# Kernel optimization log

Hardware: AMD Instinct MI355X
Metric: run time of the kernel (lower is better)

Reference implementation:

```python
import jax, jax.numpy as jnp
import numpy as np

SELF_OBS_DIM = 18
NBR_OBS_DIM = 6
NUM_NBR = 8
HID = 128

def _mlp2(x, W1, b1, W2, b2):
    return jnp.tanh(jnp.tanh(x @ W1 + b1) @ W2 + b2)

def setup_inputs() -> dict:
    key = jax.random.key(0)
    ks = jax.random.split(key, 20)
    B = 65536
    def w(k, i, o):
        return (jax.random.normal(k, (i, o), jnp.float32) / np.sqrt(i)).astype(jnp.float32)
    inp = {
        "self_obs": jax.random.normal(ks[0], (B, SELF_OBS_DIM), jnp.float32),
        "obs": jax.random.normal(ks[1], (B, SELF_OBS_DIM + NUM_NBR * NBR_OBS_DIM), jnp.float32),
        # embedding_mlp
        "e_W1": w(ks[2], SELF_OBS_DIM + NBR_OBS_DIM, HID), "e_b1": jnp.zeros((HID,), jnp.float32),
        "e_W2": w(ks[3], HID, HID), "e_b2": jnp.zeros((HID,), jnp.float32),
        # neighbor_value_mlp
        "v_W1": w(ks[4], HID, HID), "v_b1": jnp.zeros((HID,), jnp.float32),
        "v_W2": w(ks[5], HID, HID), "v_b2": jnp.zeros((HID,), jnp.float32),
        # attention_mlp
        "a_W1": w(ks[6], 2 * HID, HID), "a_b1": jnp.zeros((HID,), jnp.float32),
        "a_W2": w(ks[7], HID, HID), "a_b2": jnp.zeros((HID,), jnp.float32),
        "a_W3": w(ks[8], HID, 1), "a_b3": jnp.zeros((1,), jnp.float32),
        "all_neighbor_obs_size": NUM_NBR * NBR_OBS_DIM,
        "batch_size": B,
    }
    return inp

def reference(self_obs, obs, e_W1, e_b1, e_W2, e_b2, v_W1, v_b1, v_W2, v_b2,
              a_W1, a_b1, a_W2, a_b2, a_W3, a_b3, all_neighbor_obs_size, batch_size):
    B = batch_size
    n = NUM_NBR
    # slice out neighbor obs; reshape is batch-major: row index = b*n + k
    obs_nb = obs[:, SELF_OBS_DIM:SELF_OBS_DIM + all_neighbor_obs_size].reshape(-1, NBR_OBS_DIM)
    # torch .repeat(n, 1) tiles whole batch -> neighbor-major: row index = k*B + b (kept faithful)
    self_rep = jnp.tile(self_obs, (n, 1))
    emb = _mlp2(jnp.concatenate([self_rep, obs_nb], axis=1), e_W1, e_b1, e_W2, e_b2)  # [B*n, H]
    vals = _mlp2(emb, v_W1, v_b1, v_W2, v_b2)                                          # [B*n, H]
    emb_mean = emb.reshape(B, n, HID).mean(axis=1)                                     # [B, H]
    mean_rep = jnp.tile(emb_mean, (n, 1))                                              # [B*n, H]
    h = jnp.tanh(jnp.concatenate([emb, mean_rep], axis=1) @ a_W1 + a_b1)
    h = jnp.tanh(h @ a_W2 + a_b2)
    scores = (h @ a_W3 + a_b3).reshape(B, n)
    attn = jax.nn.softmax(scores, axis=1).reshape(-1, 1)
    out = (attn * vals).reshape(B, n, HID).sum(axis=1)                                 # [B, H]
    return out
```

## Files before the change

### kernel.cpp

```cpp
#include <hip/hip_runtime.h>
#include <math.h>

#define BATCH 65536
#define HID   128
#define NTHREADS 256

using bf16x8 = __attribute__((ext_vector_type(8))) short;
using f32x4  = __attribute__((ext_vector_type(4))) float;

#define E1H 0
#define E1L 4096
#define SWB 8192
#define BIASF 204800
#define MEANH 206592
#define WS_ELEMS_FULL (MEANH + BATCH*HID)

__device__ __forceinline__ float4 ld4(const float* p) { return *reinterpret_cast<const float4*>(p); }

__device__ __forceinline__ unsigned cvtpk(float a, float b) {
    unsigned r;
    asm("v_cvt_pk_bf16_f32 %0, %1, %2" : "=v"(r) : "v"(a), "v"(b));
    return r;
}

__device__ __forceinline__ float tanh_f(float x) {
    float t = __builtin_amdgcn_exp2f(x * 2.8853900817779268f);
    float r = __builtin_amdgcn_rcpf(t + 1.f);
    return 1.f - 2.f * r;
}

__device__ __forceinline__ f32x4 mfma16(bf16x8 a, bf16x8 b, f32x4 c) {
    return __builtin_amdgcn_mfma_f32_16x16x32_bf16(a, b, c, 0, 0, 0);
}

__device__ __forceinline__ bf16x8 pk8(unsigned u0, unsigned u1, unsigned u2, unsigned u3) {
    union { unsigned u[4]; bf16x8 v; } x;
    x.u[0] = u0; x.u[1] = u1; x.u[2] = u2; x.u[3] = u3;
    return x.v;
}

__device__ __forceinline__ void split_pack(float v0, float v1, float v2, float v3,
        unsigned& uh0, unsigned& uh1, unsigned& ul0, unsigned& ul1) {
    uh0 = cvtpk(v0, v1); uh1 = cvtpk(v2, v3);
    float f0 = __uint_as_float(uh0 << 16), f1 = __uint_as_float(uh0 & 0xffff0000u);
    float f2 = __uint_as_float(uh1 << 16), f3 = __uint_as_float(uh1 & 0xffff0000u);
    ul0 = cvtpk(v0 - f0, v1 - f1); ul1 = cvtpk(v2 - f2, v3 - f3);
}

__device__ __forceinline__ void zacc(f32x4 acc[2][8]) {
    #pragma unroll
    for (int rt = 0; rt < 2; ++rt)
        #pragma unroll
        for (int t = 0; t < 8; ++t) acc[rt][t] = f32x4{0.f, 0.f, 0.f, 0.f};
}

__device__ __forceinline__ int permc(int p) {
    return 32 * ((p >> 4) & 3) + 8 * ((p >> 2) & 3) + 4 * (p >> 6) + (p & 3);
}

__device__ __forceinline__ void gload16(const void* g, void* l) {
    __builtin_amdgcn_global_load_lds(
        (const __attribute__((address_space(1))) void*)g,
        (__attribute__((address_space(3))) void*)l, 16, 0, 0);
}
__device__ __forceinline__ void stage16k(short* dst, const short* __restrict__ src, int tid) {
    const char* g = (const char*)src + tid * 16;
    char* l = (char*)dst + tid * 16;
    #pragma unroll
    for (int s = 0; s < 4; ++s) gload16(g + s * 4096, l + s * 4096);
}
__device__ __forceinline__ void stage32k(short* dst, const short* __restrict__ src, int tid) {
    const char* g = (const char*)src + tid * 16;
    char* l = (char*)dst + tid * 16;
    #pragma unroll
    for (int s = 0; s < 8; ++s) gload16(g + s * 4096, l + s * 4096);
}

template<int NMUL, int TPH>
__device__ __forceinline__ void mm_q(f32x4 acc[2][8],
        const bf16x8 Bh[2][4], const bf16x8 Bl[2][4],
        const short* Wq, int sE, int sO)
{
    #pragma unroll
    for (int tp = 0; tp < 2; ++tp) {
        const int t0 = 4 * TPH + 2 * tp, t1 = t0 + 1;
        #pragma unroll
        for (int ks = 0; ks < 4; ++ks) {
            const int base = ((ks & 1) ? sO : sE) + (ks >> 1) * 64 + tp * 4096;
            bf16x8 w0 = *(const bf16x8*)(Wq + base);
            bf16x8 w1 = *(const bf16x8*)(Wq + base + 2048);
            __builtin_amdgcn_s_setprio(1);
            acc[0][t0] = mfma16(w0, Bh[0][ks], acc[0][t0]);
            acc[0][t1] = mfma16(w1, Bh[0][ks], acc[0][t1]);
            acc[1][t0] = mfma16(w0, Bh[1][ks], acc[1][t0]);
            acc[1][t1] = mfma16(w1, Bh[1][ks], acc[1][t1]);
            if (NMUL == 2) {
                acc[0][t0] = mfma16(w0, Bl[0][ks], acc[0][t0]);
                acc[0][t1] = mfma16(w1, Bl[0][ks], acc[0][t1]);
                acc[1][t0] = mfma16(w0, Bl[1][ks], acc[1][t0]);
                acc[1][t1] = mfma16(w1, Bl[1][ks], acc[1][t1]);
            }
            __builtin_amdgcn_s_setprio(0);
        }
    }
}

template<int NH>
__device__ __forceinline__ void layer4(f32x4 acc[2][8],
        const bf16x8 Bh[2][4], const bf16x8 Bl[2][4],
        short* B0, short* B1, const short* __restrict__ src,
        const short* __restrict__ next, int sE, int sO, int tid)
{
    stage16k(B1, src + 8192, tid);
    mm_q<NH, 0>(acc, Bh, Bl, B0, sE, sO);
    __syncthreads();
    stage16k(B0, src + 16384, tid);
    mm_q<NH, 1>(acc, Bh, Bl, B1, sE, sO);
    __syncthreads();
    stage16k(B1, src + 24576, tid);
    mm_q<1, 0>(acc, Bh, Bh, B0, sE, sO);
    __syncthreads();
    if (next) stage16k(B0, next, tid);
    mm_q<1, 1>(acc, Bh, Bh, B1, sE, sO);
}

template<int NMUL>
__device__ __forceinline__ void mm_half(f32x4 acc[2][8],
        const bf16x8 Bh[2][4], const bf16x8 Bl[2][4],
        const short* W, int sE, int sO)
{
    #pragma unroll
    for (int tp = 0; tp < 4; ++tp) {
        const int t0 = 2 * tp, t1 = t0 + 1;
        __builtin_amdgcn_s_setprio(1);
        #pragma unroll
        for (int ks = 0; ks < 4; ++ks) {
            const int base = ((ks & 1) ? sO : sE) + (ks >> 1) * 64 + tp * 4096;
            bf16x8 w0 = *(const bf16x8*)(W + base);
            bf16x8 w1 = *(const bf16x8*)(W + base + 2048);
            acc[0][t0] = mfma16(w0, Bh[0][ks], acc[0][t0]);
            acc[0][t1] = mfma16(w1, Bh[0][ks], acc[0][t1]);
            acc[1][t0] = mfma16(w0, Bh[1][ks], acc[1][t0]);
            acc[1][t1] = mfma16(w1, Bh[1][ks], acc[1][t1]);
            if (NMUL == 2) {
                acc[0][t0] = mfma16(w0, Bl[0][ks], acc[0][t0]);
                acc[0][t1] = mfma16(w1, Bl[0][ks], acc[0][t1]);
                acc[1][t0] = mfma16(w0, Bl[1][ks], acc[1][t0]);
                acc[1][t1] = mfma16(w1, Bl[1][ks], acc[1][t1]);
            }
        }
        __builtin_amdgcn_s_setprio(0);
    }
}

__device__ __forceinline__ void mm_l1(f32x4 acc[2][8],
        const bf16x8 X0h[2], const bf16x8 X0l[2],
        const short* __restrict__ Wh, const short* __restrict__ Wl, int wb)
{
    #pragma unroll
    for (int tp = 0; tp < 4; ++tp) {
        const short* whp = Wh + wb + tp * 1024;
        const short* wlp = Wl + wb + tp * 1024;
        bf16x8 wh0 = *(const bf16x8*)(whp);
        bf16x8 wh1 = *(const bf16x8*)(whp + 512);
        bf16x8 wl0 = *(const bf16x8*)(wlp);
        bf16x8 wl1 = *(const bf16x8*)(wlp + 512);
        __builtin_amdgcn_s_setprio(1);
        acc[0][2*tp  ] = mfma16(wh0, X0h[0], acc[0][2*tp  ]);
        acc[0][2*tp+1] = mfma16(wh1, X0h[0], acc[0][2*tp+1]);
        acc[1][2*tp  ] = mfma16(wh0, X0h[1], acc[1][2*tp  ]);
        acc[1][2*tp+1] = mfma16(wh1, X0h[1], acc[1][2*tp+1]);
        acc[0][2*tp  ] = mfma16(wh0, X0l[0], acc[0][2*tp  ]);
        acc[0][2*tp+1] = mfma16(wh1, X0l[0], acc[0][2*tp+1]);
        acc[1][2*tp  ] = mfma16(wh0, X0l[1], acc[1][2*tp  ]);
        acc[1][2*tp+1] = mfma16(wh1, X0l[1], acc[1][2*tp+1]);
        acc[0][2*tp  ] = mfma16(wl0, X0h[0], acc[0][2*tp  ]);
        acc[0][2*tp+1] = mfma16(wl1, X0h[0], acc[0][2*tp+1]);
        acc[1][2*tp  ] = mfma16(wl0, X0h[1], acc[1][2*tp  ]);
        acc[1][2*tp+1] = mfma16(wl1, X0h[1], acc[1][2*tp+1]);
        __builtin_amdgcn_s_setprio(0);
    }
}

__device__ __forceinline__ void epi_state(const f32x4 acc[2][8], const float* __restrict__ bp,
        int q4, bf16x8 Nh[2][4], bf16x8 Nl[2][4])
{
    #pragma unroll
    for (int ks = 0; ks < 4; ++ks) {
        float4 b0 = ld4(bp + 16 * ks + q4);
        float4 b1 = ld4(bp + 16 * ks + 64 + q4);
        #pragma unroll
        for (int rt = 0; rt < 2; ++rt) {
            unsigned h0, h1, h2, h3, l0, l1, l2, l3;
            split_pack(tanh_f(acc[rt][ks][0] + b0.x), tanh_f(acc[rt][ks][1] + b0.y),
                       tanh_f(acc[rt][ks][2] + b0.z), tanh_f(acc[rt][ks][3] + b0.w),
                       h0, h1, l0, l1);
            split_pack(tanh_f(acc[rt][ks+4][0] + b1.x), tanh_f(acc[rt][ks+4][1] + b1.y),
                       tanh_f(acc[rt][ks+4][2] + b1.z), tanh_f(acc[rt][ks+4][3] + b1.w),
                       h2, h3, l2, l3);
            Nh[rt][ks] = pk8(h0, h1, h2, h3);
            Nl[rt][ks] = pk8(l0, l1, l2, l3);
        }
    }
}

__device__ __forceinline__ void epi_state_hi(const f32x4 acc[2][8], const float* __restrict__ bp,
        int q4, bf16x8 Nh[2][4])
{
    #pragma unroll
    for (int ks = 0; ks < 4; ++ks) {
        float4 b0 = ld4(bp + 16 * ks + q4);
        float4 b1 = ld4(bp + 16 * ks + 64 + q4);
        #pragma unroll
        for (int rt = 0; rt < 2; ++rt) {
            unsigned h0 = cvtpk(tanh_f(acc[rt][ks][0] + b0.x), tanh_f(acc[rt][ks][1] + b0.y));
            unsigned h1 = cvtpk(tanh_f(acc[rt][ks][2] + b0.z), tanh_f(acc[rt][ks][3] + b0.w));
            unsigned h2 = cvtpk(tanh_f(acc[rt][ks+4][0] + b1.x), tanh_f(acc[rt][ks+4][1] + b1.y));
            unsigned h3 = cvtpk(tanh_f(acc[rt][ks+4][2] + b1.z), tanh_f(acc[rt][ks+4][3] + b1.w));
            Nh[rt][ks] = pk8(h0, h1, h2, h3);
        }
    }
}

__device__ __forceinline__ void build_x0(bf16x8 X0h[2], bf16x8 X0l[2],
        const float* __restrict__ self_obs, const float* __restrict__ obs,
        int r0w, int lm, int q)
{
    #pragma unroll
    for (int rt = 0; rt < 2; ++rt) {
        int row = r0w + 16 * rt + lm;
        const float* sp = self_obs + (size_t)(row & (BATCH - 1)) * 18;
        float x0 = 0.f, x1 = 0.f, x2 = 0.f, x3 = 0.f, x4 = 0.f, x5 = 0.f, x6 = 0.f, x7 = 0.f;
        if (q == 0) {
            x0 = sp[0]; x1 = sp[1]; x2 = sp[2]; x3 = sp[3];
            x4 = sp[4]; x5 = sp[5]; x6 = sp[6]; x7 = sp[7];
        } else if (q == 1) {
            x0 = sp[8]; x1 = sp[9]; x2 = sp[10]; x3 = sp[11];
            x4 = sp[12]; x5 = sp[13]; x6 = sp[14]; x7 = sp[15];
        } else if (q == 2) {
            x0 = sp[16]; x1 = sp[17];
            const float* op = obs + (size_t)(row >> 3) * 66 + 18 + (row & 7) * 6;
            x2 = op[0]; x3 = op[1]; x4 = op[2]; x5 = op[3]; x6 = op[4]; x7 = op[5];
        }
        unsigned h0, h1, h2, h3, l0, l1, l2, l3;
        split_pack(x0, x1, x2, x3, h0, h1, l0, l1);
        split_pack(x4, x5, x6, x7, h2, h3, l2, l3);
        X0h[rt] = pk8(h0, h1, h2, h3);
        X0l[rt] = pk8(l0, l1, l2, l3);
    }
}

__device__ __forceinline__ int remap(int hw) {
    return (((hw >> 3) & 7) << 9) | ((hw & 7) << 6) | (hw >> 6);
}

__global__ void prep_w(const float* __restrict__ eW1, const float* __restrict__ eW2,
                       const float* __restrict__ vW1, const float* __restrict__ vW2,
                       const float* __restrict__ aW1, const float* __restrict__ aW2,
                       const float* __restrict__ eb1, const float* __restrict__ eb2,
                       const float* __restrict__ vb1, const float* __restrict__ vb2,
                       const float* __restrict__ ab1, const float* __restrict__ ab2,
                       const float* __restrict__ aW3,
                       short* __restrict__ ws)
{
    int t = blockIdx.x * blockDim.x + threadIdx.x;
    if (t >= 103296) return;
    if (t >= 102400) {
        int i = t - 102400, arr = i >> 7, p = i & 127;
        int c = permc(p);
        float v;
        if      (arr == 0) v = eb1[c];
        else if (arr == 1) v = eb2[c];
        else if (arr == 2) v = vb1[c];
        else if (arr == 3) v = vb2[c];
        else if (arr == 4) v = ab1[c];
        else if (arr == 5) v = ab2[c];
        else               v = aW3[c];
        ((float*)(ws + BIASF))[arr * 128 + p] = v;
        return;
    }
    float v; int dh, dl;
    if (t < 4096) {
        int p = t >> 5, k = t & 31;
        v = (k < 24) ? eW1[k * HID + permc(p)] : 0.f;
        dh = E1H + t; dl = E1L + t;
    } else {
        int u = t - 4096;
        int blob = u >> 14, vv = u & 16383;
        int p = vv >> 7;
        int k = (vv & 127) ^ ((p & 7) << 3);
        int c = permc(p);
        if      (blob == 0) v = eW2[k * HID + c];
        else if (blob == 1) v = aW1[k * HID + c];
        else if (blob == 2) v = aW1[(128 + k) * HID + c];
        else if (blob == 3) v = aW2[k * HID + c];
        else if (blob == 4) v = vW1[k * HID + c];
        else                v = vW2[k * HID + c];
        dh = SWB + blob * 32768 + vv;
        dl = dh + 16384;
    }
    unsigned uu = __float_as_uint(v);
    unsigned h = (uu + 0x7fffu + ((uu >> 16) & 1u)) >> 16;
    float lf = v - __uint_as_float(h << 16);
    ws[dh] = (short)h;
    ws[dl] = (short)(__float_as_uint(lf) >> 16);
}

__global__ __launch_bounds__(NTHREADS, 2)
void qk_mean(const float* __restrict__ self_obs, const float* __restrict__ obs,
             short* ws)
{
    __shared__ __align__(16) short B0[8192], B1[8192];
    const int tid = threadIdx.x, lane = tid & 63;
    const int lm = lane & 15, q = lane >> 4;
    const int r0w = remap(blockIdx.x) * 128 + (tid >> 6) * 32;
    const float* bf = (const float*)(ws + BIASF);
    const int sE = (lm * 128 + 8 * q) ^ ((lm & 7) << 3);
    const int sO = (lm * 128 + 8 * q + 32) ^ ((lm & 7) << 3);

    stage16k(B0, ws + SWB, tid);

    f32x4 acc[2][8];
    bf16x8 X0h[2], X0l[2];
    build_x0(X0h, X0l, self_obs, obs, r0w, lm, q);
    zacc(acc);
    mm_l1(acc, X0h, X0l, ws + E1H, ws + E1L, lm * 32 + q * 8);
    bf16x8 Hh[2][4], Hl[2][4];
    epi_state(acc, bf, q * 4, Hh, Hl);
    __syncthreads();

    zacc(acc);
    layer4<2>(acc, Hh, Hl, B0, B1, ws + SWB, nullptr, sE, sO, tid);

    const float* b2 = bf + 128;
    short* mh = ws + MEANH;
    #pragma unroll
    for (int rt = 0; rt < 2; ++rt) {
        float m[8][4];
        #pragma unroll
        for (int ks = 0; ks < 4; ++ks) {
            float4 b0 = ld4(b2 + 16 * ks + 4 * q);
            float4 b1 = ld4(b2 + 16 * ks + 64 + 4 * q);
            m[ks][0] = tanh_f(acc[rt][ks][0] + b0.x);
            m[ks][1] = tanh_f(acc[rt][ks][1] + b0.y);
            m[ks][2] = tanh_f(acc[rt][ks][2] + b0.z);
            m[ks][3] = tanh_f(acc[rt][ks][3] + b0.w);
            m[ks+4][0] = tanh_f(acc[rt][ks+4][0] + b1.x);
            m[ks+4][1] = tanh_f(acc[rt][ks+4][1] + b1.y);
            m[ks+4][2] = tanh_f(acc[rt][ks+4][2] + b1.z);
            m[ks+4][3] = tanh_f(acc[rt][ks+4][3] + b1.w);
        }
        #pragma unroll
        for (int t = 0; t < 8; ++t)
            #pragma unroll
            for (int e = 0; e < 4; ++e) {
                float v = m[t][e];
                v += __shfl_xor(v, 1); v += __shfl_xor(v, 2); v += __shfl_xor(v, 4);
                m[t][e] = v * 0.125f;
            }
        if ((lm & 7) == 0) {
            int g = (r0w >> 3) + 2 * rt + (lm >> 3);
            #pragma unroll
            for (int ks = 0; ks < 4; ++ks) {
                unsigned h0 = cvtpk(m[ks][0], m[ks][1]);
                unsigned h1 = cvtpk(m[ks][2], m[ks][3]);
                unsigned h2 = cvtpk(m[ks+4][0], m[ks+4][1]);
                unsigned h3 = cvtpk(m[ks+4][2], m[ks+4][3]);
                *(bf16x8*)(mh + (size_t)g * 128 + 32 * ks + 8 * q) = pk8(h0, h1, h2, h3);
            }
        }
    }
}

__global__ __launch_bounds__(NTHREADS, 2)
void qk_main(const float* __restrict__ self_obs, const float* __restrict__ obs,
             short* ws, float* __restrict__ out)
{
    __shared__ __align__(16) short B0[16384], B1[16384];
    const int tid = threadIdx.x, lane = tid & 63;
    const int lm = lane & 15, q = lane >> 4;
    const int r0w = remap(blockIdx.x) * 128 + (tid >> 6) * 32;
    const float* bf = (const float*)(ws + BIASF);
    const int sE = (lm * 128 + 8 * q) ^ ((lm & 7) << 3);
    const int sO = (lm * 128 + 8 * q + 32) ^ ((lm & 7) << 3);
    const short* W = ws + SWB;

    f32x4 acc[2][8];
    float a0, a1;

    stage32k(B0, W, tid);
    {
        bf16x8 X0h[2], X0l[2];
        build_x0(X0h, X0l, self_obs, obs, r0w, lm, q);
        zacc(acc);
        mm_l1(acc, X0h, X0l, ws + E1H, ws + E1L, lm * 32 + q * 8);
    }
    bf16x8 Hh[2][4], Hl[2][4];
    epi_state(acc, bf, q * 4, Hh, Hl);
    __syncthreads();

    stage32k(B1, W + 1 * 16384, tid);
    zacc(acc);
    mm_half<2>(acc, Hh, Hl, B0, sE, sO);
    __syncthreads();
    stage32k(B0, W + 2 * 16384, tid);
    mm_half<1>(acc, Hh, Hh, B1, sE, sO);
    bf16x8 Eh[2][4], El[2][4];
    epi_state(acc, bf + 128, q * 4, Eh, El);
    __syncthreads();

    stage32k(B1, W + 3 * 16384, tid);
    zacc(acc);
    mm_half<2>(acc, Eh, El, B0, sE, sO);
    __syncthreads();
    stage32k(B0, W + 4 * 16384, tid);
    bf16x8 Mh[2][4];
    {
        const short* mh = ws + MEANH;
        const size_t mr0 = (size_t)((r0w + lm) & (BATCH - 1)) * 128;
        const size_t mr1 = (size_t)((r0w + 16 + lm) & (BATCH - 1)) * 128;
        #pragma unroll
        for (int ks = 0; ks < 4; ++ks) {
            Mh[0][ks] = *(const bf16x8*)(mh + mr0 + 32 * ks + 8 * q);
            Mh[1][ks] = *(const bf16x8*)(mh + mr1 + 32 * ks + 8 * q);
        }
    }
    mm_half<1>(acc, Eh, Eh, B1, sE, sO);
    __syncthreads();

    stage32k(B1, W + 5 * 16384, tid);
    mm_half<1>(acc, Mh, Mh, B0, sE, sO);
    __syncthreads();
    stage32k(B0, W + 6 * 16384, tid);
    mm_half<1>(acc, Mh, Mh, B1, sE, sO);
    bf16x8 Ah[2][4];
    epi_state_hi(acc, bf + 4 * 128, q * 4, Ah);
    __syncthreads();

    stage32k(B1, W + 7 * 16384, tid);
    zacc(acc);
    mm_half<1>(acc, Ah, Ah, B0, sE, sO);
    __syncthreads();
    stage32k(B0, W + 8 * 16384, tid);
    mm_half<1>(acc, Ah, Ah, B1, sE, sO);
    {
        const float* b6  = bf + 5 * 128;
        const float* w3p = bf + 6 * 128;
        float p0 = 0.f, p1 = 0.f;
        #pragma unroll
        for (int t = 0; t < 8; ++t) {
            float4 b  = ld4(b6 + 16 * t + 4 * q);
            float4 wv = ld4(w3p + 16 * t + 4 * q);
            p0 += tanh_f(acc[0][t][0] + b.x) * wv.x + tanh_f(acc[0][t][1] + b.y) * wv.y
                + tanh_f(acc[0][t][2] + b.z) * wv.z + tanh_f(acc[0][t][3] + b.w) * wv.w;
            p1 += tanh_f(acc[1][t][0] + b.x) * wv.x + tanh_f(acc[1][t][1] + b.y) * wv.y
                + tanh_f(acc[1][t][2] + b.z) * wv.z + tanh_f(acc[1][t][3] + b.w) * wv.w;
        }
        p0 += __shfl_xor(p0, 16); p0 += __shfl_xor(p0, 32);
        p1 += __shfl_xor(p1, 16); p1 += __shfl_xor(p1, 32);
        float m0 = p0, m1 = p1;
        m0 = fmaxf(m0, __shfl_xor(m0, 1)); m0 = fmaxf(m0, __shfl_xor(m0, 2)); m0 = fmaxf(m0, __shfl_xor(m0, 4));
        m1 = fmaxf(m1, __shfl_xor(m1, 1)); m1 = fmaxf(m1, __shfl_xor(m1, 2)); m1 = fmaxf(m1, __shfl_xor(m1, 4));
        float e0 = __expf(p0 - m0), e1 = __expf(p1 - m1);
        float s0 = e0, s1 = e1;
        s0 += __shfl_xor(s0, 1); s0 += __shfl_xor(s0, 2); s0 += __shfl_xor(s0, 4);
        s1 += __shfl_xor(s1, 1); s1 += __shfl_xor(s1, 2); s1 += __shfl_xor(s1, 4);
        a0 = e0 * __builtin_amdgcn_rcpf(s0);
        a1 = e1 * __builtin_amdgcn_rcpf(s1);
    }
    __syncthreads();

    stage32k(B1, W + 9 * 16384, tid);
    zacc(acc);
    mm_half<2>(acc, Eh, El, B0, sE, sO);
    __syncthreads();
    stage32k(B0, W + 10 * 16384, tid);
    mm_half<1>(acc, Eh, Eh, B1, sE, sO);
    bf16x8 Vh[2][4], Vl[2][4];
    epi_state(acc, bf + 2 * 128, q * 4, Vh, Vl);
    __syncthreads();

    stage32k(B1, W + 11 * 16384, tid);
    zacc(acc);
    mm_half<2>(acc, Vh, Vl, B0, sE, sO);
    __syncthreads();
    mm_half<1>(acc, Vh, Vh, B1, sE, sO);
    const float* b4 = bf + 3 * 128;
    #pragma unroll
    for (int rt = 0; rt < 2; ++rt) {
        const float av = rt ? a1 : a0;
        float o[8][4];
        #pragma unroll
        for (int ks = 0; ks < 4; ++ks) {
            float4 b0 = ld4(b4 + 16 * ks + 4 * q);
            float4 b1 = ld4(b4 + 16 * ks + 64 + 4 * q);
            o[ks][0] = av * tanh_f(acc[rt][ks][0] + b0.x);
            o[ks][1] = av * tanh_f(acc[rt][ks][1] + b0.y);
            o[ks][2] = av * tanh_f(acc[rt][ks][2] + b0.z);
            o[ks][3] = av * tanh_f(acc[rt][ks][3] + b0.w);
            o[ks+4][0] = av * tanh_f(acc[rt][ks+4][0] + b1.x);
            o[ks+4][1] = av * tanh_f(acc[rt][ks+4][1] + b1.y);
            o[ks+4][2] = av * tanh_f(acc[rt][ks+4][2] + b1.z);
            o[ks+4][3] = av * tanh_f(acc[rt][ks+4][3] + b1.w);
        }
        #pragma unroll
        for (int t = 0; t < 8; ++t)
            #pragma unroll
            for (int e = 0; e < 4; ++e) {
                float v = o[t][e];
                v += __shfl_xor(v, 1); v += __shfl_xor(v, 2); v += __shfl_xor(v, 4);
                o[t][e] = v;
            }
        if ((lm & 7) == 0) {
            int g = (r0w >> 3) + 2 * rt + (lm >> 3);
            #pragma unroll
            for (int ks = 0; ks < 4; ++ks) {
                *(float4*)(out + (size_t)g * 128 + 32 * ks + 8 * q) =
                    make_float4(o[ks][0], o[ks][1], o[ks][2], o[ks][3]);
                *(float4*)(out + (size_t)g * 128 + 32 * ks + 8 * q + 4) =
                    make_float4(o[ks+4][0], o[ks+4][1], o[ks+4][2], o[ks+4][3]);
            }
        }
    }
}

extern "C" void kernel_launch(void* const* d_in, const int* in_sizes, int n_in,
                              void* d_out, int out_size, void* d_ws, size_t ws_size,
                              hipStream_t stream) {
    const float* self_obs = (const float*)d_in[0];
    const float* obs      = (const float*)d_in[1];
    const float* eW1 = (const float*)d_in[2];  const float* eb1 = (const float*)d_in[3];
    const float* eW2 = (const float*)d_in[4];  const float* eb2 = (const float*)d_in[5];
    const float* vW1 = (const float*)d_in[6];  const float* vb1 = (const float*)d_in[7];
    const float* vW2 = (const float*)d_in[8];  const float* vb2 = (const float*)d_in[9];
    const float* aW1 = (const float*)d_in[10]; const float* ab1 = (const float*)d_in[11];
    const float* aW2 = (const float*)d_in[12]; const float* ab2 = (const float*)d_in[13];
    const float* aW3 = (const float*)d_in[14];
    float* out = (float*)d_out;
    short* ws = (short*)d_ws;

    prep_w<<<404, 256, 0, stream>>>(eW1, eW2, vW1, vW2, aW1, aW2,
                                    eb1, eb2, vb1, vb2, ab1, ab2, aW3, ws);

    dim3 grid(4096);
    qk_mean<<<grid, NTHREADS, 0, stream>>>(self_obs, obs, ws);
    qk_main<<<grid, NTHREADS, 0, stream>>>(self_obs, obs, ws, out);
}
```

Measured before the change: 380.1 us.

## Precompute mean-embedding attention term per batch row instead of per neighbor row

The mean embedding is identical for the 8 neighbor rows that share it, so its product with the mean half of the first attention weight is now computed once per group in the mean kernel. That kernel keeps the group means in shared memory and writes fp32 partial sums to the workspace. The main kernel loads these partials as its starting accumulator, which drops two 32k weight-stage/MMA passes per tile. In exchange the mean kernel gains extra staging and MFMA work, and the partials are fp32 where the means were bf16, so the workspace holds more data.

```diff
diff --git a/kernel.cpp b/kernel.cpp
--- a/kernel.cpp
+++ b/kernel.cpp
@@ -12,8 +12,7 @@
 #define E1L 4096
 #define SWB 8192
 #define BIASF 204800
-#define MEANH 206592
-#define WS_ELEMS_FULL (MEANH + BATCH*HID)
+#define PARTF 206592
 
 __device__ __forceinline__ float4 ld4(const float* p) { return *reinterpret_cast<const float4*>(p); }
 
@@ -109,7 +108,7 @@
 __device__ __forceinline__ void layer4(f32x4 acc[2][8],
         const bf16x8 Bh[2][4], const bf16x8 Bl[2][4],
         short* B0, short* B1, const short* __restrict__ src,
-        const short* __restrict__ next, int sE, int sO, int tid)
+        int sE, int sO, int tid)
 {
     stage16k(B1, src + 8192, tid);
     mm_q<NH, 0>(acc, Bh, Bl, B0, sE, sO);
@@ -120,7 +119,6 @@
     stage16k(B1, src + 24576, tid);
     mm_q<1, 0>(acc, Bh, Bh, B0, sE, sO);
     __syncthreads();
-    if (next) stage16k(B0, next, tid);
     mm_q<1, 1>(acc, Bh, Bh, B1, sE, sO);
 }
 
@@ -311,9 +309,10 @@
              short* ws)
 {
     __shared__ __align__(16) short B0[8192], B1[8192];
-    const int tid = threadIdx.x, lane = tid & 63;
+    __shared__ __align__(16) short MeanL[2048];
+    const int tid = threadIdx.x, lane = tid & 63, w = tid >> 6;
     const int lm = lane & 15, q = lane >> 4;
-    const int r0w = remap(blockIdx.x) * 128 + (tid >> 6) * 32;
+    const int r0w = remap(blockIdx.x) * 128 + w * 32;
     const float* bf = (const float*)(ws + BIASF);
     const int sE = (lm * 128 + 8 * q) ^ ((lm & 7) << 3);
     const int sO = (lm * 128 + 8 * q + 32) ^ ((lm & 7) << 3);
@@ -330,10 +329,9 @@
     __syncthreads();
 
     zacc(acc);
-    layer4<2>(acc, Hh, Hl, B0, B1, ws + SWB, nullptr, sE, sO, tid);
+    layer4<2>(acc, Hh, Hl, B0, B1, ws + SWB, sE, sO, tid);
 
     const float* b2 = bf + 128;
-    short* mh = ws + MEANH;
     #pragma unroll
     for (int rt = 0; rt < 2; ++rt) {
         float m[8][4];
@@ -359,16 +357,56 @@
                 m[t][e] = v * 0.125f;
             }
         if ((lm & 7) == 0) {
-            int g = (r0w >> 3) + 2 * rt + (lm >> 3);
+            int gl = 4 * w + 2 * rt + (lm >> 3);
+            int swzm = (gl & 7) << 3;
             #pragma unroll
             for (int ks = 0; ks < 4; ++ks) {
-                unsigned h0 = cvtpk(m[ks][0], m[ks][1]);
-                unsigned h1 = cvtpk(m[ks][2], m[ks][3]);
-                unsigned h2 = cvtpk(m[ks+4][0], m[ks+4][1]);
-                unsigned h3 = cvtpk(m[ks+4][2], m[ks+4][3]);
-                *(bf16x8*)(mh + (size_t)g * 128 + 32 * ks + 8 * q) = pk8(h0, h1, h2, h3);
-            }
-        }
+                unsigned u0 = cvtpk(m[ks][0], m[ks][1]);
+                unsigned u1 = cvtpk(m[ks][2], m[ks][3]);
+                unsigned u2 = cvtpk(m[ks+4][0], m[ks+4][1]);
+                unsigned u3 = cvtpk(m[ks+4][2], m[ks+4][3]);
+                *(bf16x8*)(MeanL + gl * 128 + ((32 * ks + 8 * q) ^ swzm)) = pk8(u0, u1, u2, u3);
+            }
+        }
+    }
+    __syncthreads();
+
+    {
+        const short* src = ws + SWB + 2 * 32768;
+        stage16k(B0, src, tid);
+        stage16k(B1, src + 8192, tid);
+        bf16x8 mB[4];
+        #pragma unroll
+        for (int ks = 0; ks < 4; ++ks)
+            mB[ks] = *(const bf16x8*)(MeanL + ((ks & 1) ? sO : sE) + (ks >> 1) * 64);
+        const short* Bw = (w < 2) ? B0 : B1;
+        const int wq = (w & 1) * 4096;
+        f32x4 p0 = f32x4{0.f, 0.f, 0.f, 0.f}, p1 = f32x4{0.f, 0.f, 0.f, 0.f};
+        __syncthreads();
+        #pragma unroll
+        for (int ks = 0; ks < 4; ++ks) {
+            const int base = wq + ((ks & 1) ? sO : sE) + (ks >> 1) * 64;
+            bf16x8 w0 = *(const bf16x8*)(Bw + base);
+            bf16x8 w1 = *(const bf16x8*)(Bw + base + 2048);
+            p0 = mfma16(w0, mB[ks], p0);
+            p1 = mfma16(w1, mB[ks], p1);
+        }
+        __syncthreads();
+        stage16k(B0, src + 16384, tid);
+        stage16k(B1, src + 16384 + 8192, tid);
+        __syncthreads();
+        #pragma unroll
+        for (int ks = 0; ks < 4; ++ks) {
+            const int base = wq + ((ks & 1) ? sO : sE) + (ks >> 1) * 64;
+            bf16x8 w0 = *(const bf16x8*)(Bw + base);
+            bf16x8 w1 = *(const bf16x8*)(Bw + base + 2048);
+            p0 = mfma16(w0, mB[ks], p0);
+            p1 = mfma16(w1, mB[ks], p1);
+        }
+        float* part = (float*)(ws + PARTF);
+        size_t b = (size_t)((r0w >> 3) - 4 * w + lm);
+        *(float4*)(part + b * 128 + 32 * w + 4 * q) = make_float4(p0[0], p0[1], p0[2], p0[3]);
+        *(float4*)(part + b * 128 + 32 * w + 16 + 4 * q) = make_float4(p1[0], p1[1], p1[2], p1[3]);
     }
 }
 
@@ -388,7 +426,7 @@
     f32x4 acc[2][8];
     float a0, a1;
 
-    stage32k(B0, W, tid);
+    stage32k(B0, W + 0 * 16384, tid);
     {
         bf16x8 X0h[2], X0l[2];
         build_x0(X0h, X0l, self_obs, obs, r0w, lm, q);
@@ -409,30 +447,23 @@
     epi_state(acc, bf + 128, q * 4, Eh, El);
     __syncthreads();
 
+    {
+        const float* part = (const float*)(ws + PARTF);
+        #pragma unroll
+        for (int rt = 0; rt < 2; ++rt) {
+            size_t b = (size_t)((r0w + rt * 16 + lm) & (BATCH - 1));
+            #pragma unroll
+            for (int t = 0; t < 8; ++t) {
+                float4 pv = ld4(part + b * 128 + 16 * t + 4 * q);
+                acc[rt][t] = f32x4{pv.x, pv.y, pv.z, pv.w};
+            }
+        }
+    }
     stage32k(B1, W + 3 * 16384, tid);
-    zacc(acc);
     mm_half<2>(acc, Eh, El, B0, sE, sO);
     __syncthreads();
-    stage32k(B0, W + 4 * 16384, tid);
-    bf16x8 Mh[2][4];
-    {
-        const short* mh = ws + MEANH;
-        const size_t mr0 = (size_t)((r0w + lm) & (BATCH - 1)) * 128;
-        const size_t mr1 = (size_t)((r0w + 16 + lm) & (BATCH - 1)) * 128;
-        #pragma unroll
-        for (int ks = 0; ks < 4; ++ks) {
-            Mh[0][ks] = *(const bf16x8*)(mh + mr0 + 32 * ks + 8 * q);
-            Mh[1][ks] = *(const bf16x8*)(mh + mr1 + 32 * ks + 8 * q);
-        }
-    }
+    stage32k(B0, W + 6 * 16384, tid);
     mm_half<1>(acc, Eh, Eh, B1, sE, sO);
-    __syncthreads();
-
-    stage32k(B1, W + 5 * 16384, tid);
-    mm_half<1>(acc, Mh, Mh, B0, sE, sO);
-    __syncthreads();
-    stage32k(B0, W + 6 * 16384, tid);
-    mm_half<1>(acc, Mh, Mh, B1, sE, sO);
     bf16x8 Ah[2][4];
     epi_state_hi(acc, bf + 4 * 128, q * 4, Ah);
     __syncthreads();
```

Result: no change. 377.6 us (-0.7%).
